# Kernel tuning notes

Measured on AMD Instinct MI355X. Metric: run time of the kernel, lower is better.

Reference implementation:

```python
import jax, jax.numpy as jnp
import numpy as np

B, NPG, E_PER = 64, 1024, 16384   # graphs per batch, nodes per graph, edges per graph
IN, HID, OUT = 64, 128, 32
N = B * NPG


def setup_inputs() -> dict:
    key = jax.random.key(0)
    ks = jax.random.split(key, 10)
    off = (jnp.arange(B, dtype=jnp.int32) * NPG)[:, None]
    # block-diagonal edges (DGL batched graph: edges stay within each subgraph)
    src = (jax.random.randint(ks[0], (B, E_PER), 0, NPG, jnp.int32) + off).reshape(-1)
    dst = (jax.random.randint(ks[1], (B, E_PER), 0, NPG, jnp.int32) + off).reshape(-1)
    features = jax.random.normal(ks[2], (N, IN), jnp.float32)
    noise = jax.random.normal(ks[3], (N, OUT), jnp.float32)
    glorot = lambda k, i, o: jax.random.normal(k, (i, o), jnp.float32) * np.sqrt(2.0 / (i + o))
    return {
        'features': features, 'src': src, 'dst': dst, 'noise': noise,
        'W1': glorot(ks[4], IN, HID),  'b1': jnp.zeros((HID,), jnp.float32),
        'W2': glorot(ks[5], HID, OUT), 'b2': jnp.zeros((OUT,), jnp.float32),
        'W3': glorot(ks[6], HID, OUT), 'b3': jnp.zeros((OUT,), jnp.float32),
    }


def _gconv(h, src, dst, W, b, n):
    # DGL GraphConv, norm='both': D_out^{-1/2} scale, sum-aggregate src->dst, D_in^{-1/2} scale, linear
    ones = jnp.ones(src.shape[0], h.dtype)
    deg_out = jnp.maximum(jax.ops.segment_sum(ones, src, num_segments=n), 1.0)
    deg_in = jnp.maximum(jax.ops.segment_sum(ones, dst, num_segments=n), 1.0)
    h = h * jax.lax.rsqrt(deg_out)[:, None]
    m = jax.ops.segment_sum(h[src], dst, num_segments=n)   # irregular gather + scatter-add
    m = m * jax.lax.rsqrt(deg_in)[:, None]
    return m @ W + b


def reference(features, src, dst, noise, W1, b1, W2, b2, W3, b3):
    n = features.shape[0]
    h = jax.nn.relu(_gconv(features, src, dst, W1, b1, n))
    mean = _gconv(h, src, dst, W2, b2, n)
    log_std = _gconv(h, src, dst, W3, b3, n)
    z = mean + noise * jnp.exp(log_std)                    # reparameterization
    zb = z.reshape(B, NPG, OUT)
    adj_rec = jax.nn.sigmoid(jnp.einsum('bnd,bmd->bnm', zb, zb))  # per-graph sigmoid(z z^T)
    return adj_rec, mean.reshape(B, NPG, OUT), log_std.reshape(B, NPG, OUT)
```

## Files before the change

### kernel.cpp

```cpp
#include <hip/hip_runtime.h>

constexpr int NB   = 64;
constexpr int NPG  = 1024;
constexpr int EPG  = 16384;
constexpr int NTOT = NB * NPG;
constexpr int ETOT = NB * EPG;
constexpr int FIN  = 64;
constexpr int FHID = 128;
constexpr int FOUT = 32;

__global__ __launch_bounds__(1024) void k_deg(
    const int* __restrict__ src, const int* __restrict__ dst,
    int* __restrict__ dego, int* __restrict__ degi) {
  __shared__ int so[NPG], si[NPG];
  const int g = blockIdx.x, q = blockIdx.y;
  for (int i = threadIdx.x; i < NPG; i += 1024) { so[i] = 0; si[i] = 0; }
  __syncthreads();
  const int eb = g * EPG + q * (EPG / 4);
  const int gb = g * NPG;
  for (int e = threadIdx.x; e < EPG / 4; e += 1024) {
    atomicAdd(&so[src[eb + e] - gb], 1);
    atomicAdd(&si[dst[eb + e] - gb], 1);
  }
  __syncthreads();
  for (int i = threadIdx.x; i < NPG; i += 1024) {
    if (so[i]) atomicAdd(&dego[gb + i], so[i]);
    if (si[i]) atomicAdd(&degi[gb + i], si[i]);
  }
}

__global__ void k_scales(const int* __restrict__ dego, const int* __restrict__ degi,
                         float* __restrict__ rso, float* __restrict__ rsi) {
  int i = blockIdx.x * blockDim.x + threadIdx.x;
  if (i < NTOT) {
    int a = dego[i] > 1 ? dego[i] : 1;
    int b = degi[i] > 1 ? degi[i] : 1;
    rso[i] = rsqrtf((float)a);
    rsi[i] = rsqrtf((float)b);
  }
}

__global__ __launch_bounds__(1024) void k_scan(
    const int* __restrict__ degi, int* __restrict__ ptr, int* __restrict__ cursor) {
  __shared__ int s[NPG];
  const int g = blockIdx.x, t = threadIdx.x;
  const int d = degi[g * NPG + t];
  s[t] = d;
  __syncthreads();
  for (int off = 1; off < NPG; off <<= 1) {
    int v = (t >= off) ? s[t - off] : 0;
    __syncthreads();
    s[t] += v;
    __syncthreads();
  }
  const int p = g * EPG + (s[t] - d);
  ptr[g * NPG + t] = p;
  cursor[g * NPG + t] = p;
  if (g == 0 && t == 0) ptr[NTOT] = ETOT;
}

__global__ void k_fill(const int* __restrict__ src, const int* __restrict__ dst,
                       int* __restrict__ cursor, int* __restrict__ csr) {
  int e = blockIdx.x * blockDim.x + threadIdx.x;
  if (e < ETOT) {
    int d = dst[e];
    int pos = atomicAdd(&cursor[d], 1);
    csr[pos] = src[e];
  }
}

__global__ void k_prefold(const float* __restrict__ features,
                          const int* __restrict__ dego, float* __restrict__ x1) {
  int t = blockIdx.x * blockDim.x + threadIdx.x;
  int node = t >> 4, q = t & 15;
  int dg = dego[node];
  float sc = rsqrtf((float)(dg > 1 ? dg : 1));
  float4 v = *(const float4*)&features[(size_t)node * FIN + q * 4];
  v.x *= sc; v.y *= sc; v.z *= sc; v.w *= sc;
  *(float4*)&x1[(size_t)node * FIN + q * 4] = v;
}

__global__ __launch_bounds__(256) void k_agg_csr(
    const int* __restrict__ ptr, const int* __restrict__ csr,
    const float* __restrict__ x, const float* __restrict__ rsi,
    float* __restrict__ out) {
  const int nblk = gridDim.x;
  const int bid  = blockIdx.x;
  const int swz  = (bid & 7) * (nblk >> 3) + (bid >> 3);
  const int node = swz * 4 + (threadIdx.x >> 6);
  const int lane = threadIdx.x & 63;

  const int start = ptr[node];
  const int end   = ptr[node + 1];
  const int deg   = end - start;

  float acc = 0.0f;
  const float* xb = x + lane;
  if (deg > 0) {
    const int jm = deg < 64 ? deg : 64;
    const int idxv = csr[start + (lane < jm ? lane : 0)];
    for (int j = 0; j < jm; j += 8) {
      int   sj[8];
      float vj[8];
#pragma unroll
      for (int u = 0; u < 8; ++u) {
        int l = j + u;
        sj[u] = __builtin_amdgcn_readlane(idxv, l < jm ? l : 0);
      }
#pragma unroll
      for (int u = 0; u < 8; ++u) vj[u] = xb[(size_t)sj[u] * FIN];
#pragma unroll
      for (int u = 0; u < 8; ++u) acc += (j + u < jm) ? vj[u] : 0.0f;
    }
    for (int e = start + 64; e < end; ++e) acc += xb[(size_t)csr[e] * FIN];
  }
  out[(size_t)node * FIN + lane] = acc * rsi[node];
}

__global__ __launch_bounds__(256) void k_gemm1(
    const float* __restrict__ m1, const float* __restrict__ rso,
    const float* __restrict__ W1, const float* __restrict__ b1,
    float* __restrict__ h) {
  __shared__ float sA[FIN][64];
  __shared__ float sW[FIN * FHID];
  __shared__ float sB[FHID];
  const int t = threadIdx.x;
  const int node0 = blockIdx.x * 64;
  for (int f = t; f < FIN * FHID / 4; f += 256)
    ((float4*)sW)[f] = ((const float4*)W1)[f];
  if (t < FHID) sB[t] = b1[t];
  for (int f = t; f < 64 * (FIN / 4); f += 256) {
    int node = f & 63, kq = f >> 6;
    size_t idx = (size_t)(node0 + node) * FIN + kq * 4;
    float4 va = *(const float4*)&m1[idx];
    sA[kq * 4 + 0][node] = va.x;
    sA[kq * 4 + 1][node] = va.y;
    sA[kq * 4 + 2][node] = va.z;
    sA[kq * 4 + 3][node] = va.w;
  }
  __syncthreads();
  const int tx = t & 15, ty = t >> 4;
  float acc[4][8];
#pragma unroll
  for (int r = 0; r < 4; ++r)
#pragma unroll
    for (int c = 0; c < 8; ++c) acc[r][c] = 0.0f;
#pragma unroll 4
  for (int k = 0; k < FIN; ++k) {
    float4 a  = *(float4*)&sA[k][ty * 4];
    float4 w0 = *(float4*)&sW[k * FHID + tx * 8];
    float4 w1 = *(float4*)&sW[k * FHID + tx * 8 + 4];
    float av[4] = {a.x, a.y, a.z, a.w};
    float wv[8] = {w0.x, w0.y, w0.z, w0.w, w1.x, w1.y, w1.z, w1.w};
#pragma unroll
    for (int r = 0; r < 4; ++r)
#pragma unroll
      for (int c = 0; c < 8; ++c) acc[r][c] = fmaf(av[r], wv[c], acc[r][c]);
  }
#pragma unroll
  for (int r = 0; r < 4; ++r) {
    int node = node0 + ty * 4 + r;
    float sc = rso[node];
    float4 o0, o1;
    o0.x = fmaxf(acc[r][0] + sB[tx * 8 + 0], 0.f) * sc;
    o0.y = fmaxf(acc[r][1] + sB[tx * 8 + 1], 0.f) * sc;
    o0.z = fmaxf(acc[r][2] + sB[tx * 8 + 2], 0.f) * sc;
    o0.w = fmaxf(acc[r][3] + sB[tx * 8 + 3], 0.f) * sc;
    o1.x = fmaxf(acc[r][4] + sB[tx * 8 + 4], 0.f) * sc;
    o1.y = fmaxf(acc[r][5] + sB[tx * 8 + 5], 0.f) * sc;
    o1.z = fmaxf(acc[r][6] + sB[tx * 8 + 6], 0.f) * sc;
    o1.w = fmaxf(acc[r][7] + sB[tx * 8 + 7], 0.f) * sc;
    *(float4*)&h[(size_t)node * FHID + tx * 8]     = o0;
    *(float4*)&h[(size_t)node * FHID + tx * 8 + 4] = o1;
  }
}

__global__ __launch_bounds__(256) void k_gemm2(
    const float* __restrict__ h, const float* __restrict__ W2,
    const float* __restrict__ W3, float* __restrict__ p) {
  __shared__ float sA[FHID][64];
  __shared__ float sW[FHID * 64];
  const int t = threadIdx.x;
  const int node0 = blockIdx.x * 64;
  for (int f = t; f < FHID * FOUT / 4; f += 256) {
    int k = f >> 3, jq = f & 7;
    *(float4*)&sW[k * 64 + jq * 4]      = *(const float4*)&W2[k * FOUT + jq * 4];
  }
  for (int f = t; f < FHID * FOUT / 4; f += 256) {
    int k = f >> 3, jq = f & 7;
    *(float4*)&sW[k * 64 + 32 + jq * 4] = *(const float4*)&W3[k * FOUT + jq * 4];
  }
  for (int f = t; f < 64 * (FHID / 4); f += 256) {
    int node = f & 63, kq = f >> 6;
    float4 v = *(const float4*)&h[(size_t)(node0 + node) * FHID + kq * 4];
    sA[kq * 4 + 0][node] = v.x;
    sA[kq * 4 + 1][node] = v.y;
    sA[kq * 4 + 2][node] = v.z;
    sA[kq * 4 + 3][node] = v.w;
  }
  __syncthreads();
  const int tx = t & 15, ty = t >> 4;
  float acc[4][4];
#pragma unroll
  for (int r = 0; r < 4; ++r)
#pragma unroll
    for (int c = 0; c < 4; ++c) acc[r][c] = 0.0f;
#pragma unroll 4
  for (int k = 0; k < FHID; ++k) {
    float4 a = *(float4*)&sA[k][ty * 4];
    float4 w = *(float4*)&sW[k * 64 + tx * 4];
    float av[4] = {a.x, a.y, a.z, a.w};
    float wv[4] = {w.x, w.y, w.z, w.w};
#pragma unroll
    for (int r = 0; r < 4; ++r)
#pragma unroll
      for (int c = 0; c < 4; ++c) acc[r][c] = fmaf(av[r], wv[c], acc[r][c]);
  }
#pragma unroll
  for (int r = 0; r < 4; ++r) {
    float4 o = {acc[r][0], acc[r][1], acc[r][2], acc[r][3]};
    *(float4*)&p[(size_t)(node0 + ty * 4 + r) * 64 + tx * 4] = o;
  }
}

__global__ void k_epi(const float* __restrict__ m2,
                      const float* __restrict__ b2, const float* __restrict__ b3,
                      float* __restrict__ mean_, float* __restrict__ logstd_) {
  int t = blockIdx.x * blockDim.x + threadIdx.x;
  int node = t >> 3, q = t & 7;
  size_t im = (size_t)node * 64 + q * 4;
  size_t il = im + 32;
  float4 ma = *(const float4*)&m2[im];
  float4 la = *(const float4*)&m2[il];
  float4 bb2 = *(const float4*)&b2[q * 4];
  float4 bb3 = *(const float4*)&b3[q * 4];
  float4 me = {ma.x + bb2.x, ma.y + bb2.y, ma.z + bb2.z, ma.w + bb2.w};
  float4 ls = {la.x + bb3.x, la.y + bb3.y, la.z + bb3.z, la.w + bb3.w};
  *(float4*)&mean_[(size_t)node * FOUT + q * 4]   = me;
  *(float4*)&logstd_[(size_t)node * FOUT + q * 4] = ls;
}

__global__ __launch_bounds__(256) void k_adj(
    const float* __restrict__ mean_, const float* __restrict__ logstd_,
    const float* __restrict__ noise, float* __restrict__ adj) {
  __shared__ float sR[FOUT][128];
  __shared__ float sC[FOUT][128];
  const int g  = blockIdx.z;
  const int c0 = blockIdx.x * 128;
  const int r0 = blockIdx.y * 128;
  const int t  = threadIdx.x;
  const size_t gb = (size_t)g * NPG;
  for (int f = t; f < 2048; f += 256) {
    int half = f >> 10;
    int ff   = f & 1023;
    int node = ff & 127, kq = ff >> 7;
    int base = half ? c0 : r0;
    size_t idx = (gb + base + node) * FOUT + kq * 4;
    float4 m  = *(const float4*)&mean_[idx];
    float4 l  = *(const float4*)&logstd_[idx];
    float4 nz = *(const float4*)&noise[idx];
    float* s = half ? &sC[0][0] : &sR[0][0];
    s[(kq * 4 + 0) * 128 + node] = m.x + nz.x * __expf(l.x);
    s[(kq * 4 + 1) * 128 + node] = m.y + nz.y * __expf(l.y);
    s[(kq * 4 + 2) * 128 + node] = m.z + nz.z * __expf(l.z);
    s[(kq * 4 + 3) * 128 + node] = m.w + nz.w * __expf(l.w);
  }
  __syncthreads();
  const int tx = t & 15, ty = t >> 4;
  float acc[8][8];
#pragma unroll
  for (int r = 0; r < 8; ++r)
#pragma unroll
    for (int c = 0; c < 8; ++c) acc[r][c] = 0.0f;
#pragma unroll 2
  for (int k = 0; k < FOUT; ++k) {
    float ar[8], ac[8];
    *(float4*)&ar[0] = *(float4*)&sR[k][ty * 8];
    *(float4*)&ar[4] = *(float4*)&sR[k][ty * 8 + 4];
    *(float4*)&ac[0] = *(float4*)&sC[k][tx * 8];
    *(float4*)&ac[4] = *(float4*)&sC[k][tx * 8 + 4];
#pragma unroll
    for (int r = 0; r < 8; ++r)
#pragma unroll
      for (int c = 0; c < 8; ++c) acc[r][c] = fmaf(ar[r], ac[c], acc[r][c]);
  }
#pragma unroll
  for (int r = 0; r < 8; ++r) {
    size_t o = (gb + r0 + ty * 8 + r) * (size_t)NPG + c0 + tx * 8;
    float4 s0, s1;
    s0.x = 1.0f / (1.0f + __expf(-acc[r][0]));
    s0.y = 1.0f / (1.0f + __expf(-acc[r][1]));
    s0.z = 1.0f / (1.0f + __expf(-acc[r][2]));
    s0.w = 1.0f / (1.0f + __expf(-acc[r][3]));
    s1.x = 1.0f / (1.0f + __expf(-acc[r][4]));
    s1.y = 1.0f / (1.0f + __expf(-acc[r][5]));
    s1.z = 1.0f / (1.0f + __expf(-acc[r][6]));
    s1.w = 1.0f / (1.0f + __expf(-acc[r][7]));
    *(float4*)&adj[o]     = s0;
    *(float4*)&adj[o + 4] = s1;
  }
}

extern "C" void kernel_launch(void* const* d_in, const int* in_sizes, int n_in,
                              void* d_out, int out_size, void* d_ws, size_t ws_size,
                              hipStream_t stream) {
  const float* features = (const float*)d_in[0];
  const int*   src      = (const int*)d_in[1];
  const int*   dst      = (const int*)d_in[2];
  const float* noise    = (const float*)d_in[3];
  const float* W1       = (const float*)d_in[4];
  const float* b1       = (const float*)d_in[5];
  const float* W2       = (const float*)d_in[6];
  const float* b2       = (const float*)d_in[7];
  const float* W3       = (const float*)d_in[8];
  const float* b3       = (const float*)d_in[9];

  float* adj     = (float*)d_out;
  float* mean_   = adj + (size_t)NB * NPG * NPG;
  float* logstd_ = mean_ + (size_t)NTOT * FOUT;

  float* x1   = adj;
  float* m1   = x1 + (size_t)NTOT * FIN;
  float* h    = m1 + (size_t)NTOT * FIN;
  float* p    = h + (size_t)NTOT * FHID;
  float* m2   = p + (size_t)NTOT * FIN;
  int*   dego = (int*)(m2 + (size_t)NTOT * FIN);
  int*   degi = dego + NTOT;
  float* rso  = (float*)(degi + NTOT);
  float* rsi  = rso + NTOT;
  int*   ptr  = (int*)(rsi + NTOT);
  int*   cur  = ptr + (NTOT + 1);
  int*   csr  = cur + NTOT;

  hipMemsetAsync(dego, 0, (size_t)2 * NTOT * sizeof(int), stream);
  k_deg<<<dim3(NB, 4), 1024, 0, stream>>>(src, dst, dego, degi);
  k_scales<<<NTOT / 256, 256, 0, stream>>>(dego, degi, rso, rsi);
  k_scan<<<NB, 1024, 0, stream>>>(degi, ptr, cur);
  k_fill<<<ETOT / 256, 256, 0, stream>>>(src, dst, cur, csr);
  k_prefold<<<NTOT * 16 / 256, 256, 0, stream>>>(features, dego, x1);
  k_agg_csr<<<NTOT / 4, 256, 0, stream>>>(ptr, csr, x1, rsi, m1);
  k_gemm1<<<NTOT / 64, 256, 0, stream>>>(m1, rso, W1, b1, h);
  k_gemm2<<<NTOT / 64, 256, 0, stream>>>(h, W2, W3, p);
  k_agg_csr<<<NTOT / 4, 256, 0, stream>>>(ptr, csr, p, rsi, m2);
  k_epi<<<NTOT * 8 / 256, 256, 0, stream>>>(m2, b2, b3, mean_, logstd_);
  k_adj<<<dim3(NPG / 128, NPG / 128, NB), 256, 0, stream>>>(mean_, logstd_, noise, adj);
}
```

Before: 547.9 us.

## Fuse bias epilogue into second aggregation and rework adj tile column mapping

Measured after the change: 528.7 us. -3.5%, faster.

```diff
diff --git a/kernel.cpp b/kernel.cpp
--- a/kernel.cpp
+++ b/kernel.cpp
@@ -115,6 +115,47 @@
     for (int e = start + 64; e < end; ++e) acc += xb[(size_t)csr[e] * FIN];
   }
   out[(size_t)node * FIN + lane] = acc * rsi[node];
+}
+
+__global__ __launch_bounds__(256) void k_agg2(
+    const int* __restrict__ ptr, const int* __restrict__ csr,
+    const float* __restrict__ x, const float* __restrict__ rsi,
+    const float* __restrict__ b2, const float* __restrict__ b3,
+    float* __restrict__ mean_, float* __restrict__ logstd_) {
+  const int nblk = gridDim.x;
+  const int bid  = blockIdx.x;
+  const int swz  = (bid & 7) * (nblk >> 3) + (bid >> 3);
+  const int node = swz * 4 + (threadIdx.x >> 6);
+  const int lane = threadIdx.x & 63;
+
+  const int start = ptr[node];
+  const int end   = ptr[node + 1];
+  const int deg   = end - start;
+
+  float acc = 0.0f;
+  const float* xb = x + lane;
+  if (deg > 0) {
+    const int jm = deg < 64 ? deg : 64;
+    const int idxv = csr[start + (lane < jm ? lane : 0)];
+    for (int j = 0; j < jm; j += 8) {
+      int   sj[8];
+      float vj[8];
+#pragma unroll
+      for (int u = 0; u < 8; ++u) {
+        int l = j + u;
+        sj[u] = __builtin_amdgcn_readlane(idxv, l < jm ? l : 0);
+      }
+#pragma unroll
+      for (int u = 0; u < 8; ++u) vj[u] = xb[(size_t)sj[u] * FIN];
+#pragma unroll
+      for (int u = 0; u < 8; ++u) acc += (j + u < jm) ? vj[u] : 0.0f;
+    }
+    for (int e = start + 64; e < end; ++e) acc += xb[(size_t)csr[e] * FIN];
+  }
+  const float bias = (lane < FOUT) ? b2[lane] : b3[lane - FOUT];
+  const float v = acc * rsi[node] + bias;
+  if (lane < FOUT) mean_[(size_t)node * FOUT + lane] = v;
+  else             logstd_[(size_t)node * FOUT + (lane - FOUT)] = v;
 }
 
 __global__ __launch_bounds__(256) void k_gemm1(
@@ -221,23 +262,6 @@
     float4 o = {acc[r][0], acc[r][1], acc[r][2], acc[r][3]};
     *(float4*)&p[(size_t)(node0 + ty * 4 + r) * 64 + tx * 4] = o;
   }
-}
-
-__global__ void k_epi(const float* __restrict__ m2,
-                      const float* __restrict__ b2, const float* __restrict__ b3,
-                      float* __restrict__ mean_, float* __restrict__ logstd_) {
-  int t = blockIdx.x * blockDim.x + threadIdx.x;
-  int node = t >> 3, q = t & 7;
-  size_t im = (size_t)node * 64 + q * 4;
-  size_t il = im + 32;
-  float4 ma = *(const float4*)&m2[im];
-  float4 la = *(const float4*)&m2[il];
-  float4 bb2 = *(const float4*)&b2[q * 4];
-  float4 bb3 = *(const float4*)&b3[q * 4];
-  float4 me = {ma.x + bb2.x, ma.y + bb2.y, ma.z + bb2.z, ma.w + bb2.w};
-  float4 ls = {la.x + bb3.x, la.y + bb3.y, la.z + bb3.z, la.w + bb3.w};
-  *(float4*)&mean_[(size_t)node * FOUT + q * 4]   = me;
-  *(float4*)&logstd_[(size_t)node * FOUT + q * 4] = ls;
 }
 
 __global__ __launch_bounds__(256) void k_adj(
@@ -274,30 +298,31 @@
     for (int c = 0; c < 8; ++c) acc[r][c] = 0.0f;
 #pragma unroll 2
   for (int k = 0; k < FOUT; ++k) {
-    float ar[8], ac[8];
-    *(float4*)&ar[0] = *(float4*)&sR[k][ty * 8];
-    *(float4*)&ar[4] = *(float4*)&sR[k][ty * 8 + 4];
-    *(float4*)&ac[0] = *(float4*)&sC[k][tx * 8];
-    *(float4*)&ac[4] = *(float4*)&sC[k][tx * 8 + 4];
+    float4 a0 = *(const float4*)&sR[k][ty * 8];
+    float4 a1 = *(const float4*)&sR[k][ty * 8 + 4];
+    float4 q0 = *(const float4*)&sC[k][tx * 4];
+    float4 q1 = *(const float4*)&sC[k][tx * 4 + 64];
+    float av[8] = {a0.x, a0.y, a0.z, a0.w, a1.x, a1.y, a1.z, a1.w};
+    float cv[8] = {q0.x, q0.y, q0.z, q0.w, q1.x, q1.y, q1.z, q1.w};
 #pragma unroll
     for (int r = 0; r < 8; ++r)
 #pragma unroll
-      for (int c = 0; c < 8; ++c) acc[r][c] = fmaf(ar[r], ac[c], acc[r][c]);
+      for (int c = 0; c < 8; ++c) acc[r][c] = fmaf(av[r], cv[c], acc[r][c]);
   }
 #pragma unroll
   for (int r = 0; r < 8; ++r) {
-    size_t o = (gb + r0 + ty * 8 + r) * (size_t)NPG + c0 + tx * 8;
+    size_t row = gb + r0 + ty * 8 + r;
     float4 s0, s1;
-    s0.x = 1.0f / (1.0f + __expf(-acc[r][0]));
-    s0.y = 1.0f / (1.0f + __expf(-acc[r][1]));
-    s0.z = 1.0f / (1.0f + __expf(-acc[r][2]));
-    s0.w = 1.0f / (1.0f + __expf(-acc[r][3]));
-    s1.x = 1.0f / (1.0f + __expf(-acc[r][4]));
-    s1.y = 1.0f / (1.0f + __expf(-acc[r][5]));
-    s1.z = 1.0f / (1.0f + __expf(-acc[r][6]));
-    s1.w = 1.0f / (1.0f + __expf(-acc[r][7]));
-    *(float4*)&adj[o]     = s0;
-    *(float4*)&adj[o + 4] = s1;
+    s0.x = __builtin_amdgcn_rcpf(1.0f + __expf(-acc[r][0]));
+    s0.y = __builtin_amdgcn_rcpf(1.0f + __expf(-acc[r][1]));
+    s0.z = __builtin_amdgcn_rcpf(1.0f + __expf(-acc[r][2]));
+    s0.w = __builtin_amdgcn_rcpf(1.0f + __expf(-acc[r][3]));
+    s1.x = __builtin_amdgcn_rcpf(1.0f + __expf(-acc[r][4]));
+    s1.y = __builtin_amdgcn_rcpf(1.0f + __expf(-acc[r][5]));
+    s1.z = __builtin_amdgcn_rcpf(1.0f + __expf(-acc[r][6]));
+    s1.w = __builtin_amdgcn_rcpf(1.0f + __expf(-acc[r][7]));
+    *(float4*)&adj[row * NPG + c0 + tx * 4]      = s0;
+    *(float4*)&adj[row * NPG + c0 + 64 + tx * 4] = s1;
   }
 }
 
@@ -323,8 +348,7 @@
   float* m1   = x1 + (size_t)NTOT * FIN;
   float* h    = m1 + (size_t)NTOT * FIN;
   float* p    = h + (size_t)NTOT * FHID;
-  float* m2   = p + (size_t)NTOT * FIN;
-  int*   dego = (int*)(m2 + (size_t)NTOT * FIN);
+  int*   dego = (int*)(p + (size_t)NTOT * FIN);
   int*   degi = dego + NTOT;
   float* rso  = (float*)(degi + NTOT);
   float* rsi  = rso + NTOT;
@@ -341,7 +365,6 @@
   k_agg_csr<<<NTOT / 4, 256, 0, stream>>>(ptr, csr, x1, rsi, m1);
   k_gemm1<<<NTOT / 64, 256, 0, stream>>>(m1, rso, W1, b1, h);
   k_gemm2<<<NTOT / 64, 256, 0, stream>>>(h, W2, W3, p);
-  k_agg_csr<<<NTOT / 4, 256, 0, stream>>>(ptr, csr, p, rsi, m2);
-  k_epi<<<NTOT * 8 / 256, 256, 0, stream>>>(m2, b2, b3, mean_, logstd_);
+  k_agg2<<<NTOT / 4, 256, 0, stream>>>(ptr, csr, p, rsi, b2, b3, mean_, logstd_);
   k_adj<<<dim3(NPG / 128, NPG / 128, NB), 256, 0, stream>>>(mean_, logstd_, noise, adj);
 }
```
